# Kernel optimization log

Hardware: AMD Instinct MI355X
Metric: run time of the kernel (lower is better)

The kernel has to match this reference:

```python
import jax, jax.numpy as jnp
import numpy as np

DIM = 1024
HEADS = 16
HEAD_DIM = DIM // HEADS
HIDDEN = 4 * DIM
SCALE = HEAD_DIM ** -0.5
EPS = 1e-5


def _layernorm(x, g, b):
    mu = jnp.mean(x, axis=-1, keepdims=True)
    var = jnp.mean(jnp.square(x - mu), axis=-1, keepdims=True)
    return (x - mu) * jax.lax.rsqrt(var + EPS) * g + b


def setup_inputs() -> dict:
    key = jax.random.key(0)
    ks = jax.random.split(key, 8)
    B, N, C = 4, 2048, DIM
    s = 0.02
    return {
        "x": jax.random.normal(ks[0], (B, N, C), dtype=jnp.float32),
        "ln1_g": jnp.ones((C,), jnp.float32),
        "ln1_b": jnp.zeros((C,), jnp.float32),
        "qkv_w": jax.random.normal(ks[1], (3 * C, C), jnp.float32) * s,
        "proj_w": jax.random.normal(ks[2], (C, C), jnp.float32) * s,
        "proj_b": jnp.zeros((C,), jnp.float32),
        "ln2_g": jnp.ones((C,), jnp.float32),
        "ln2_b": jnp.zeros((C,), jnp.float32),
        "fc1_w": jax.random.normal(ks[3], (HIDDEN, C), jnp.float32) * s,
        "fc1_b": jnp.zeros((HIDDEN,), jnp.float32),
        "fc2_w": jax.random.normal(ks[4], (C, HIDDEN), jnp.float32) * s,
        "fc2_b": jnp.zeros((C,), jnp.float32),
    }


def reference(x, ln1_g, ln1_b, qkv_w, proj_w, proj_b, ln2_g, ln2_b, fc1_w, fc1_b, fc2_w, fc2_b):
    B, N, C = x.shape
    # --- attention branch ---
    h = _layernorm(x, ln1_g, ln1_b)
    qkv = h @ qkv_w.T                                  # [B,N,3C]
    qkv = qkv.reshape(B, N, 3, HEADS, HEAD_DIM)
    q = qkv[:, :, 0].transpose(0, 2, 1, 3) * SCALE      # [B,H,N,D]
    k = qkv[:, :, 1].transpose(0, 2, 1, 3)
    v = qkv[:, :, 2].transpose(0, 2, 1, 3)
    attn = jax.nn.softmax(jnp.einsum('bhqd,bhkd->bhqk', q, k), axis=-1)
    o = jnp.einsum('bhqk,bhkd->bhqd', attn, v)          # [B,H,N,D]
    o = o.transpose(0, 2, 1, 3).reshape(B, N, C)
    x = x + (o @ proj_w.T + proj_b)
    # --- MLP branch ---
    h2 = _layernorm(x, ln2_g, ln2_b)
    h2 = jax.nn.gelu(h2 @ fc1_w.T + fc1_b, approximate=False)
    x = x + (h2 @ fc2_w.T + fc2_b)
    return x
```

## Files before the change

kernel.cpp:

```cpp
#include <hip/hip_runtime.h>
#include <math.h>

typedef __bf16 bf16;
typedef __attribute__((ext_vector_type(8))) __bf16 bf16x8;
typedef __attribute__((ext_vector_type(4))) __bf16 bf16x4;
typedef __attribute__((ext_vector_type(4))) float floatx4;

#define MFMA(a, b, c) __builtin_amdgcn_mfma_f32_16x16x32_bf16((a), (b), (c), 0, 0, 0)

__device__ __forceinline__ void async_load16(const bf16* g, bf16* l) {
    __builtin_amdgcn_global_load_lds((const __attribute__((address_space(1))) void*)(g),
                                     (__attribute__((address_space(3))) void*)(l), 16, 0, 0);
}

__global__ __launch_bounds__(256) void cast_kernel(const float* __restrict__ in,
                                                   bf16* __restrict__ out, int n8) {
    int i = blockIdx.x * 256 + threadIdx.x;
    if (i >= n8) return;
    const float4 a = ((const float4*)in)[2 * i];
    const float4 b = ((const float4*)in)[2 * i + 1];
    bf16x8 o;
    o[0] = (bf16)a.x; o[1] = (bf16)a.y; o[2] = (bf16)a.z; o[3] = (bf16)a.w;
    o[4] = (bf16)b.x; o[5] = (bf16)b.y; o[6] = (bf16)b.z; o[7] = (bf16)b.w;
    *(bf16x8*)(out + (long)i * 8) = o;
}

__global__ __launch_bounds__(256) void ln_kernel(const float* __restrict__ x,
                                                 const float* __restrict__ g,
                                                 const float* __restrict__ b,
                                                 bf16* __restrict__ out) {
    const int row = blockIdx.x;
    const int tid = threadIdx.x;
    const float4 v = ((const float4*)(x + (long)row * 1024))[tid];
    float s  = v.x + v.y + v.z + v.w;
    float s2 = v.x * v.x + v.y * v.y + v.z * v.z + v.w * v.w;
#pragma unroll
    for (int off = 32; off > 0; off >>= 1) {
        s  += __shfl_xor(s, off, 64);
        s2 += __shfl_xor(s2, off, 64);
    }
    __shared__ float red[8];
    const int wave = tid >> 6, lane = tid & 63;
    if (lane == 0) { red[wave] = s; red[wave + 4] = s2; }
    __syncthreads();
    const float ts  = red[0] + red[1] + red[2] + red[3];
    const float ts2 = red[4] + red[5] + red[6] + red[7];
    const float mu   = ts * (1.0f / 1024.0f);
    const float rstd = rsqrtf(ts2 * (1.0f / 1024.0f) - mu * mu + 1e-5f);
    const float4 gg = ((const float4*)g)[tid];
    const float4 bb = ((const float4*)b)[tid];
    bf16x4 o;
    o[0] = (bf16)((v.x - mu) * rstd * gg.x + bb.x);
    o[1] = (bf16)((v.y - mu) * rstd * gg.y + bb.y);
    o[2] = (bf16)((v.z - mu) * rstd * gg.z + bb.z);
    o[3] = (bf16)((v.w - mu) * rstd * gg.w + bb.w);
    *(bf16x4*)(out + (long)row * 1024 + tid * 4) = o;
}

template <int EPI>
__global__ __launch_bounds__(256, 2)
void gemm_bt(const bf16* __restrict__ A, const bf16* __restrict__ B,
             const float* __restrict__ bias, const float* __restrict__ resid,
             void* __restrict__ Cout, int M, int N, int K) {
    __shared__ __align__(16) bf16 sA[128 * 64];
    __shared__ __align__(16) bf16 sB[128 * 64];
    const int tid  = threadIdx.x;
    const int lane = tid & 63;
    const int wave = tid >> 6;
    const int wm = (wave >> 1) << 6;
    const int wn = (wave & 1) << 6;
    const int c15 = lane & 15;
    const int kq  = lane >> 4;
    const int c7  = lane & 7;
    const long tileM = (long)blockIdx.y * 128;
    const long tileN = (long)blockIdx.x * 128;

    floatx4 acc[4][4] = {};

    const int srow = tid >> 3;
    const int scol = ((tid & 7) ^ (srow & 7)) * 8;
    const bf16* Abase = A + (tileM + srow) * (long)K + scol;
    const bf16* Bbase = B + (tileN + srow) * (long)K + scol;
    bf16* sAw = sA + tid * 8;
    bf16* sBw = sB + tid * 8;

    for (int k0 = 0; k0 < K; k0 += 64) {
        __syncthreads();
#pragma unroll
        for (int it = 0; it < 4; ++it) {
            async_load16(Abase + (long)it * 32 * K + k0, sAw + it * 2048);
            async_load16(Bbase + (long)it * 32 * K + k0, sBw + it * 2048);
        }
        __syncthreads();
#pragma unroll
        for (int kk = 0; kk < 2; ++kk) {
            bf16x8 a[4], b[4];
#pragma unroll
            for (int i = 0; i < 4; ++i) {
                const int ch = ((kk << 2) + kq) ^ c7;
                a[i] = *(const bf16x8*)(sA + (wm + i * 16 + c15) * 64 + ch * 8);
                b[i] = *(const bf16x8*)(sB + (wn + i * 16 + c15) * 64 + ch * 8);
            }
#pragma unroll
            for (int i = 0; i < 4; ++i)
#pragma unroll
                for (int j = 0; j < 4; ++j)
                    acc[i][j] = MFMA(a[i], b[j], acc[i][j]);
        }
    }

#pragma unroll
    for (int i = 0; i < 4; ++i)
#pragma unroll
        for (int j = 0; j < 4; ++j)
#pragma unroll
            for (int r = 0; r < 4; ++r) {
                const long gm = tileM + wm + i * 16 + kq * 4 + r;
                const long gn = tileN + wn + j * 16 + c15;
                const float v = acc[i][j][r];
                if (EPI == 0) {
                    ((bf16*)Cout)[gm * N + gn] = (bf16)v;
                } else if (EPI == 1) {
                    ((float*)Cout)[gm * N + gn] = v + bias[gn] + resid[gm * N + gn];
                } else {
                    const float t = v + bias[gn];
                    ((bf16*)Cout)[gm * N + gn] =
                        (bf16)(0.5f * t * (1.0f + erff(t * 0.70710678118654752f)));
                }
            }
}

__global__ __launch_bounds__(256) void vtrans_kernel(const bf16* __restrict__ qkv,
                                                     bf16* __restrict__ vt) {
    __shared__ __align__(16) bf16 sT[64 * 72];
    const int bh = blockIdx.y;
    const int kv0 = blockIdx.x * 64;
    const int b = bh >> 4, h = bh & 15;
    const int tid = threadIdx.x;
#pragma unroll
    for (int it = 0; it < 2; ++it) {
        const int l = it * 256 + tid;
        const int row = l >> 3, c = (l & 7) * 8;
        const bf16x8 v =
            *(const bf16x8*)(qkv + ((long)(b * 2048 + kv0 + row)) * 3072 + 2048 + h * 64 + c);
        *(bf16x8*)(sT + row * 72 + c) = v;
    }
    __syncthreads();
    const int d = tid >> 2;
    const int vc = (tid & 3) * 8;
#pragma unroll
    for (int half = 0; half < 2; ++half) {
        const int kvl = half * 32 + vc;
        bf16x8 o;
#pragma unroll
        for (int jj = 0; jj < 8; ++jj) o[jj] = sT[(kvl + jj) * 72 + d];
        *(bf16x8*)(vt + ((long)bh * 64 + d) * 2048 + kv0 + kvl) = o;
    }
}

__global__ __launch_bounds__(256, 4)
void attn_kernel(const bf16* __restrict__ qkv, const bf16* __restrict__ vt,
                 bf16* __restrict__ o) {
    __shared__ __align__(16) bf16 sK[64 * 64];
    __shared__ __align__(16) bf16 sV[64 * 64];
    __shared__ __align__(16) bf16 sP[8][16 * 72];
    const int bh = blockIdx.x, b = bh >> 4, h = bh & 15;
    const int q0 = blockIdx.y * 128;
    const int tid = threadIdx.x, lane = tid & 63, wave = tid >> 6;
    const int c15 = lane & 15, kq = lane >> 4, c7 = lane & 7;

    bf16x8 qf[2][2];
#pragma unroll
    for (int t = 0; t < 2; ++t) {
        const bf16* qrow =
            qkv + ((long)(b * 2048 + q0 + wave * 32 + t * 16 + c15)) * 3072 + h * 64;
#pragma unroll
        for (int kk = 0; kk < 2; ++kk) {
            const bf16x8 raw = *(const bf16x8*)(qrow + kk * 32 + kq * 8);
            bf16x8 sc;
#pragma unroll
            for (int e = 0; e < 8; ++e) sc[e] = (bf16)((float)raw[e] * 0.18033688f);
            qf[t][kk] = sc;
        }
    }

    floatx4 oacc[2][4] = {};
    float l_s[2] = {0.f, 0.f};

    const bf16* kbase = qkv + ((long)b * 2048) * 3072 + 1024 + h * 64;
    const bf16* vbase = vt + (long)bh * 64 * 2048;

    const int srow = tid >> 3;
    const int scol = ((tid & 7) ^ (srow & 7)) * 8;
    bf16* sKw = sK + tid * 8;
    bf16* sVw = sV + tid * 8;
    bf16* sP0 = sP[wave * 2];
    bf16* sP1 = sP[wave * 2 + 1];

    for (int kv0 = 0; kv0 < 2048; kv0 += 64) {
        __syncthreads();
#pragma unroll
        for (int it = 0; it < 2; ++it) {
            async_load16(kbase + (long)(kv0 + it * 32 + srow) * 3072 + scol, sKw + it * 2048);
            async_load16(vbase + (long)(it * 32 + srow) * 2048 + kv0 + scol, sVw + it * 2048);
        }
        __syncthreads();

        floatx4 s0[4], s1[4];
#pragma unroll
        for (int j = 0; j < 4; ++j) {
            const bf16x8 k0 = *(const bf16x8*)(sK + (j * 16 + c15) * 64 + ((kq ^ c7) * 8));
            const bf16x8 k1 = *(const bf16x8*)(sK + (j * 16 + c15) * 64 + (((4 | kq) ^ c7) * 8));
            floatx4 a0 = {0.f, 0.f, 0.f, 0.f}, a1 = {0.f, 0.f, 0.f, 0.f};
            a0 = MFMA(k0, qf[0][0], a0);
            a0 = MFMA(k1, qf[0][1], a0);
            a1 = MFMA(k0, qf[1][0], a1);
            a1 = MFMA(k1, qf[1][1], a1);
            s0[j] = a0;
            s1[j] = a1;
        }

#pragma unroll
        for (int t = 0; t < 2; ++t) {
            floatx4* s = (t == 0) ? s0 : s1;
            bf16* sPt = (t == 0) ? sP0 : sP1;
            float rs = 0.f;
#pragma unroll
            for (int j = 0; j < 4; ++j) {
                const float p0 = __builtin_amdgcn_exp2f(s[j][0]);
                const float p1 = __builtin_amdgcn_exp2f(s[j][1]);
                const float p2 = __builtin_amdgcn_exp2f(s[j][2]);
                const float p3 = __builtin_amdgcn_exp2f(s[j][3]);
                rs += (p0 + p1) + (p2 + p3);
                bf16x4 pk;
                pk[0] = (bf16)p0; pk[1] = (bf16)p1; pk[2] = (bf16)p2; pk[3] = (bf16)p3;
                *(bf16x4*)(sPt + c15 * 72 + j * 16 + kq * 4) = pk;
            }
            l_s[t] += rs;
        }

        bf16x8 pf[2][2];
#pragma unroll
        for (int t = 0; t < 2; ++t) {
            bf16* sPt = (t == 0) ? sP0 : sP1;
            pf[t][0] = *(const bf16x8*)(sPt + c15 * 72 + kq * 8);
            pf[t][1] = *(const bf16x8*)(sPt + c15 * 72 + 32 + kq * 8);
        }
#pragma unroll
        for (int i = 0; i < 4; ++i) {
            const bf16x8 v0 = *(const bf16x8*)(sV + (i * 16 + c15) * 64 + ((kq ^ c7) * 8));
            const bf16x8 v1 = *(const bf16x8*)(sV + (i * 16 + c15) * 64 + (((4 | kq) ^ c7) * 8));
            oacc[0][i] = MFMA(v0, pf[0][0], oacc[0][i]);
            oacc[0][i] = MFMA(v1, pf[0][1], oacc[0][i]);
            oacc[1][i] = MFMA(v0, pf[1][0], oacc[1][i]);
            oacc[1][i] = MFMA(v1, pf[1][1], oacc[1][i]);
        }
    }

#pragma unroll
    for (int t = 0; t < 2; ++t) {
        float rs = l_s[t];
        rs += __shfl_xor(rs, 16, 64);
        rs += __shfl_xor(rs, 32, 64);
        const float linv = 1.0f / rs;
        const long tok = (long)(b * 2048 + q0 + wave * 32 + t * 16 + c15);
#pragma unroll
        for (int i = 0; i < 4; ++i) {
            bf16x4 ov;
#pragma unroll
            for (int r = 0; r < 4; ++r) ov[r] = (bf16)(oacc[t][i][r] * linv);
            *(bf16x4*)(o + tok * 1024 + h * 64 + i * 16 + kq * 4) = ov;
        }
    }
}

extern "C" void kernel_launch(void* const* d_in, const int* in_sizes, int n_in,
                              void* d_out, int out_size, void* d_ws, size_t ws_size,
                              hipStream_t stream) {
    const float* x      = (const float*)d_in[0];
    const float* ln1_g  = (const float*)d_in[1];
    const float* ln1_b  = (const float*)d_in[2];
    const float* qkv_w  = (const float*)d_in[3];
    const float* proj_w = (const float*)d_in[4];
    const float* proj_b = (const float*)d_in[5];
    const float* ln2_g  = (const float*)d_in[6];
    const float* ln2_b  = (const float*)d_in[7];
    const float* fc1_w  = (const float*)d_in[8];
    const float* fc1_b  = (const float*)d_in[9];
    const float* fc2_w  = (const float*)d_in[10];
    const float* fc2_b  = (const float*)d_in[11];
    float* out = (float*)d_out;

    char* ws = (char*)d_ws;
    bf16* actbuf = (bf16*)(ws);
    bf16* wqkv   = (bf16*)(ws + (16ull << 20));
    bf16* wproj  = (bf16*)(ws + (22ull << 20));
    bf16* wfc1   = (bf16*)(ws + (24ull << 20));
    bf16* wfc2   = (bf16*)(ws + (32ull << 20));
    bf16* qkvbuf = (bf16*)(ws + (40ull << 20));
    bf16* vtbuf  = (bf16*)(ws + (88ull << 20));
    bf16* gbuf   = (bf16*)(ws + (40ull << 20));

    const dim3 blk(256);

    cast_kernel<<<1536, blk, 0, stream>>>(qkv_w, wqkv, 3072 * 1024 / 8);
    cast_kernel<<<512,  blk, 0, stream>>>(proj_w, wproj, 1024 * 1024 / 8);
    cast_kernel<<<2048, blk, 0, stream>>>(fc1_w, wfc1, 4096 * 1024 / 8);
    cast_kernel<<<2048, blk, 0, stream>>>(fc2_w, wfc2, 4096 * 1024 / 8);

    ln_kernel<<<8192, blk, 0, stream>>>(x, ln1_g, ln1_b, actbuf);

    gemm_bt<0><<<dim3(24, 64), blk, 0, stream>>>(actbuf, wqkv, nullptr, nullptr,
                                                 qkvbuf, 8192, 3072, 1024);
    vtrans_kernel<<<dim3(32, 64), blk, 0, stream>>>(qkvbuf, vtbuf);
    attn_kernel<<<dim3(64, 16), blk, 0, stream>>>(qkvbuf, vtbuf, actbuf);

    gemm_bt<1><<<dim3(8, 64), blk, 0, stream>>>(actbuf, wproj, proj_b, x,
                                                d_out, 8192, 1024, 1024);

    ln_kernel<<<8192, blk, 0, stream>>>(out, ln2_g, ln2_b, actbuf);

    gemm_bt<2><<<dim3(32, 64), blk, 0, stream>>>(actbuf, wfc1, fc1_b, nullptr,
                                                 gbuf, 8192, 4096, 1024);
    gemm_bt<1><<<dim3(8, 64), blk, 0, stream>>>(gbuf, wfc2, fc2_b, out,
                                                d_out, 8192, 1024, 4096);
}
```

Before: 518.2 us.

## Fuse V transpose into QKV GEMM epilogue, merge weight casts, raise GEMM occupancy

The QKV GEMM epilogue now writes the V columns directly in transposed layout into the vt buffer, which removes the separate vtrans kernel and its extra read and write of V. The four weight-cast launches are merged into one kernel that picks its source by index range. GEMM launch bounds are raised to three blocks per CU, which limits registers per thread and may cause spills with 64 accumulators. The transposed stores are 8-byte writes strided by 2048 elements, so they are less coalesced than the old path.

New measurement: 496.6 us. 4.2% less time.

```diff
diff --git a/kernel.cpp b/kernel.cpp
--- a/kernel.cpp
+++ b/kernel.cpp
@@ -13,16 +13,28 @@
                                      (__attribute__((address_space(3))) void*)(l), 16, 0, 0);
 }
 
-__global__ __launch_bounds__(256) void cast_kernel(const float* __restrict__ in,
-                                                   bf16* __restrict__ out, int n8) {
-    int i = blockIdx.x * 256 + threadIdx.x;
-    if (i >= n8) return;
-    const float4 a = ((const float4*)in)[2 * i];
-    const float4 b = ((const float4*)in)[2 * i + 1];
+__global__ __launch_bounds__(256) void cast4_kernel(const float* __restrict__ a0,
+                                                    const float* __restrict__ a1,
+                                                    const float* __restrict__ a2,
+                                                    const float* __restrict__ a3,
+                                                    bf16* __restrict__ o0,
+                                                    bf16* __restrict__ o1,
+                                                    bf16* __restrict__ o2,
+                                                    bf16* __restrict__ o3) {
+    long i = (long)blockIdx.x * 256 + threadIdx.x;
+    const float* in;
+    bf16* out;
+    long off;
+    if (i < 393216) { in = a0; out = o0; off = i; }
+    else if (i < 524288) { in = a1; out = o1; off = i - 393216; }
+    else if (i < 1048576) { in = a2; out = o2; off = i - 524288; }
+    else { in = a3; out = o3; off = i - 1048576; }
+    const float4 a = ((const float4*)in)[2 * off];
+    const float4 b = ((const float4*)in)[2 * off + 1];
     bf16x8 o;
     o[0] = (bf16)a.x; o[1] = (bf16)a.y; o[2] = (bf16)a.z; o[3] = (bf16)a.w;
     o[4] = (bf16)b.x; o[5] = (bf16)b.y; o[6] = (bf16)b.z; o[7] = (bf16)b.w;
-    *(bf16x8*)(out + (long)i * 8) = o;
+    *(bf16x8*)(out + off * 8) = o;
 }
 
 __global__ __launch_bounds__(256) void ln_kernel(const float* __restrict__ x,
@@ -58,10 +70,10 @@
 }
 
 template <int EPI>
-__global__ __launch_bounds__(256, 2)
+__global__ __launch_bounds__(256, 3)
 void gemm_bt(const bf16* __restrict__ A, const bf16* __restrict__ B,
              const float* __restrict__ bias, const float* __restrict__ resid,
-             void* __restrict__ Cout, int M, int N, int K) {
+             void* __restrict__ Cout, bf16* __restrict__ vtout, int M, int N, int K) {
     __shared__ __align__(16) bf16 sA[128 * 64];
     __shared__ __align__(16) bf16 sB[128 * 64];
     const int tid  = threadIdx.x;
@@ -112,50 +124,33 @@
 #pragma unroll
     for (int i = 0; i < 4; ++i)
 #pragma unroll
-        for (int j = 0; j < 4; ++j)
-#pragma unroll
-            for (int r = 0; r < 4; ++r) {
-                const long gm = tileM + wm + i * 16 + kq * 4 + r;
-                const long gn = tileN + wn + j * 16 + c15;
-                const float v = acc[i][j][r];
-                if (EPI == 0) {
-                    ((bf16*)Cout)[gm * N + gn] = (bf16)v;
-                } else if (EPI == 1) {
-                    ((float*)Cout)[gm * N + gn] = v + bias[gn] + resid[gm * N + gn];
-                } else {
-                    const float t = v + bias[gn];
-                    ((bf16*)Cout)[gm * N + gn] =
-                        (bf16)(0.5f * t * (1.0f + erff(t * 0.70710678118654752f)));
+        for (int j = 0; j < 4; ++j) {
+            if (EPI == 3 && tileN >= 2048) {
+                const long gnv  = tileN - 2048 + wn + j * 16 + c15;
+                const long tokb = tileM + wm + i * 16 + kq * 4;
+                const long row  = ((tokb >> 11) << 10) + gnv;
+                bf16x4 ov;
+#pragma unroll
+                for (int r = 0; r < 4; ++r) ov[r] = (bf16)acc[i][j][r];
+                *(bf16x4*)(vtout + row * 2048 + (tokb & 2047)) = ov;
+            } else {
+#pragma unroll
+                for (int r = 0; r < 4; ++r) {
+                    const long gm = tileM + wm + i * 16 + kq * 4 + r;
+                    const long gn = tileN + wn + j * 16 + c15;
+                    const float v = acc[i][j][r];
+                    if (EPI == 0 || EPI == 3) {
+                        ((bf16*)Cout)[gm * N + gn] = (bf16)v;
+                    } else if (EPI == 1) {
+                        ((float*)Cout)[gm * N + gn] = v + bias[gn] + resid[gm * N + gn];
+                    } else {
+                        const float t = v + bias[gn];
+                        ((bf16*)Cout)[gm * N + gn] =
+                            (bf16)(0.5f * t * (1.0f + erff(t * 0.70710678118654752f)));
+                    }
                 }
             }
-}
-
-__global__ __launch_bounds__(256) void vtrans_kernel(const bf16* __restrict__ qkv,
-                                                     bf16* __restrict__ vt) {
-    __shared__ __align__(16) bf16 sT[64 * 72];
-    const int bh = blockIdx.y;
-    const int kv0 = blockIdx.x * 64;
-    const int b = bh >> 4, h = bh & 15;
-    const int tid = threadIdx.x;
-#pragma unroll
-    for (int it = 0; it < 2; ++it) {
-        const int l = it * 256 + tid;
-        const int row = l >> 3, c = (l & 7) * 8;
-        const bf16x8 v =
-            *(const bf16x8*)(qkv + ((long)(b * 2048 + kv0 + row)) * 3072 + 2048 + h * 64 + c);
-        *(bf16x8*)(sT + row * 72 + c) = v;
-    }
-    __syncthreads();
-    const int d = tid >> 2;
-    const int vc = (tid & 3) * 8;
-#pragma unroll
-    for (int half = 0; half < 2; ++half) {
-        const int kvl = half * 32 + vc;
-        bf16x8 o;
-#pragma unroll
-        for (int jj = 0; jj < 8; ++jj) o[jj] = sT[(kvl + jj) * 72 + d];
-        *(bf16x8*)(vt + ((long)bh * 64 + d) * 2048 + kv0 + kvl) = o;
-    }
+        }
 }
 
 __global__ __launch_bounds__(256, 4)
@@ -303,25 +298,22 @@
 
     const dim3 blk(256);
 
-    cast_kernel<<<1536, blk, 0, stream>>>(qkv_w, wqkv, 3072 * 1024 / 8);
-    cast_kernel<<<512,  blk, 0, stream>>>(proj_w, wproj, 1024 * 1024 / 8);
-    cast_kernel<<<2048, blk, 0, stream>>>(fc1_w, wfc1, 4096 * 1024 / 8);
-    cast_kernel<<<2048, blk, 0, stream>>>(fc2_w, wfc2, 4096 * 1024 / 8);
+    cast4_kernel<<<6144, blk, 0, stream>>>(qkv_w, proj_w, fc1_w, fc2_w,
+                                           wqkv, wproj, wfc1, wfc2);
 
     ln_kernel<<<8192, blk, 0, stream>>>(x, ln1_g, ln1_b, actbuf);
 
-    gemm_bt<0><<<dim3(24, 64), blk, 0, stream>>>(actbuf, wqkv, nullptr, nullptr,
-                                                 qkvbuf, 8192, 3072, 1024);
-    vtrans_kernel<<<dim3(32, 64), blk, 0, stream>>>(qkvbuf, vtbuf);
+    gemm_bt<3><<<dim3(24, 64), blk, 0, stream>>>(actbuf, wqkv, nullptr, nullptr,
+                                                 qkvbuf, vtbuf, 8192, 3072, 1024);
     attn_kernel<<<dim3(64, 16), blk, 0, stream>>>(qkvbuf, vtbuf, actbuf);
 
     gemm_bt<1><<<dim3(8, 64), blk, 0, stream>>>(actbuf, wproj, proj_b, x,
-                                                d_out, 8192, 1024, 1024);
+                                                d_out, nullptr, 8192, 1024, 1024);
 
     ln_kernel<<<8192, blk, 0, stream>>>(out, ln2_g, ln2_b, actbuf);
 
     gemm_bt<2><<<dim3(32, 64), blk, 0, stream>>>(actbuf, wfc1, fc1_b, nullptr,
-                                                 gbuf, 8192, 4096, 1024);
+                                                 gbuf, nullptr, 8192, 4096, 1024);
     gemm_bt<1><<<dim3(8, 64), blk, 0, stream>>>(gbuf, wfc2, fc2_b, out,
-                                                d_out, 8192, 1024, 4096);
-}
+                                                d_out, nullptr, 8192, 1024, 4096);
+}
```
